# Performance work log

Hardware: AMD Instinct MI355X
Metric: run time of the kernel (lower is better)

Reference implementation:

```python
import jax, jax.numpy as jnp
import numpy as np

B, T, N, D, H, MH = 4, 16, 128, 16, 64, 128  # batch, timesteps, nodes, n_in_node, n_hid, msg_hid


def setup_inputs() -> dict:
    key = jax.random.key(0)
    ks = jax.random.split(key, 24)
    s = 0.1
    inp = {
        'A': jax.random.uniform(ks[0], (B, N, N), dtype=jnp.float32),
        'X': jax.random.normal(ks[1], (B, T, N, D), dtype=jnp.float32),
        'W_msg1': s * jax.random.normal(ks[2], (2 * H, MH), dtype=jnp.float32),
        'b_msg1': s * jax.random.normal(ks[3], (MH,), dtype=jnp.float32),
        'W_msg2': s * jax.random.normal(ks[4], (MH, H), dtype=jnp.float32),
        'b_msg2': s * jax.random.normal(ks[5], (H,), dtype=jnp.float32),
        'W_ir': s * jax.random.normal(ks[6], (D, H), dtype=jnp.float32),
        'b_ir': s * jax.random.normal(ks[7], (H,), dtype=jnp.float32),
        'W_ii': s * jax.random.normal(ks[8], (D, H), dtype=jnp.float32),
        'b_ii': s * jax.random.normal(ks[9], (H,), dtype=jnp.float32),
        'W_in': s * jax.random.normal(ks[10], (D, H), dtype=jnp.float32),
        'b_in': s * jax.random.normal(ks[11], (H,), dtype=jnp.float32),
        'W_hr': s * jax.random.normal(ks[12], (H, H), dtype=jnp.float32),
        'W_hi': s * jax.random.normal(ks[13], (H, H), dtype=jnp.float32),
        'W_hh': s * jax.random.normal(ks[14], (H, H), dtype=jnp.float32),
        'W_o1': s * jax.random.normal(ks[15], (H, H), dtype=jnp.float32),
        'b_o1': s * jax.random.normal(ks[16], (H,), dtype=jnp.float32),
        'W_o2': s * jax.random.normal(ks[17], (H, H), dtype=jnp.float32),
        'b_o2': s * jax.random.normal(ks[18], (H,), dtype=jnp.float32),
        'W_o3': s * jax.random.normal(ks[19], (H, D), dtype=jnp.float32),
        'b_o3': s * jax.random.normal(ks[20], (D,), dtype=jnp.float32),
        'log_sigma': jnp.log(jnp.float32(0.1)),
    }
    return inp


def reference(A, X, W_msg1, b_msg1, W_msg2, b_msg2, W_ir, b_ir, W_ii, b_ii,
              W_in, b_in, W_hr, W_hi, W_hh, W_o1, b_o1, W_o2, b_o2, W_o3,
              b_o3, log_sigma):
    Bv, Tv, Nv, Dv = X.shape
    Hv = W_hr.shape[0]
    # project_adjacency: symmetrize, zero diag, clamp to [0,1]
    A = (A + jnp.swapaxes(A, -1, -2)) * 0.5
    A = A * (1.0 - jnp.eye(Nv, dtype=A.dtype))
    A = jnp.clip(A, 0.0, 1.0)
    # split msg_fc1 into sender / receiver halves (cat([senders, receivers]) @ W)
    W1s, W1r = W_msg1[:Hv], W_msg1[Hv:]

    def step(carry, xs):
        hidden, total = carry
        x_t, x_next = xs  # [B,N,D]
        # message passing on hidden state: msg1[b,i,j] = tanh(h_i@W1s + h_j@W1r + b)
        hs = hidden @ W1s                      # [B,N,MH] sender part
        hr = hidden @ W1r + b_msg1             # [B,N,MH] receiver part
        m1 = jnp.tanh(hs[:, :, None, :] + hr[:, None, :, :])  # [B,N,N,MH]
        msg = jnp.tanh(m1 @ W_msg2 + b_msg2)   # [B,N,N,H]
        # weight by soft adjacency, sum over senders i -> agg at receiver j
        agg = jnp.einsum('bij,bijh->bjh', A, msg)  # [B,N,H]
        # GRU-style gating
        r = jax.nn.sigmoid(x_t @ W_ir + b_ir + agg @ W_hr)
        i = jax.nn.sigmoid(x_t @ W_ii + b_ii + agg @ W_hi)
        n = jnp.tanh(x_t @ W_in + b_in + r * (agg @ W_hh))
        hidden_new = (1.0 - i) * n + i * hidden
        # output MLP with residual
        p1 = jax.nn.relu(hidden_new @ W_o1 + b_o1)
        p2 = jax.nn.relu(p1 @ W_o2 + b_o2)
        pred = x_t + (p2 @ W_o3 + b_o3)
        # gaussian log-likelihood
        sigma = jnp.exp(log_sigma)
        mse = jnp.sum((x_next - pred) ** 2)
        const = Nv * Dv * Bv * jnp.log(sigma * jnp.sqrt(2.0 * jnp.pi))
        total = total - (mse / (2.0 * sigma ** 2) + const)
        return (hidden_new, total), pred

    hidden0 = jnp.zeros((Bv, Nv, Hv), dtype=X.dtype)
    xs = (jnp.swapaxes(X[:, :-1], 0, 1), jnp.swapaxes(X[:, 1:], 0, 1))  # time-major
    (_, loglik), preds = jax.lax.scan(step, (hidden0, jnp.float32(0.0)), xs)
    X_pred = jnp.swapaxes(preds, 0, 1)  # [B, T-1, N, D]
    return X_pred, loglik
```

## Files before the change

### kernel.cpp

```cpp
#include <hip/hip_runtime.h>

#define NBLK 512
#define CSCALE 2.8853900817779268f

#define OFF_HS   0
#define OFF_PART 65536
#define OFF_SYNC 66048
#define OFF_BF   66560

#define BW2F  0
#define BWIR  8192
#define BWII  9216
#define BWIN  10240
#define BWHR  11264
#define BWHI  15360
#define BWHH  19456
#define BWO1  23552
#define BWO2  27648
#define BWO3  31744
#define BW1S  32768
#define BW1RT 49152

#define INIT_TOTAL (32768 + 512 + 49152 + 8192)

typedef __attribute__((ext_vector_type(8))) __bf16 bf16x8;
typedef __attribute__((ext_vector_type(4))) float f32x4;
union frag_u { bf16x8 v; unsigned short s[8]; int4 q; };
union ldu { int4 q; unsigned short s[8]; unsigned u[4]; };

__device__ __forceinline__ unsigned short f2b(float x) {
  unsigned int u = __float_as_uint(x);
  u += 0x7fffu + ((u >> 16) & 1u);
  return (unsigned short)(u >> 16);
}
__device__ __forceinline__ float b2f(unsigned short u) {
  return __uint_as_float(((unsigned int)u) << 16);
}
__device__ __forceinline__ float fast_tanh(float x) {
  float e = __builtin_amdgcn_exp2f(x * CSCALE);
  return 1.0f - 2.0f * __builtin_amdgcn_rcpf(e + 1.0f);
}
__device__ __forceinline__ float tanh_pre(float x) {
  float e = __builtin_amdgcn_exp2f(x);
  return 1.0f - 2.0f * __builtin_amdgcn_rcpf(e + 1.0f);
}
__device__ __forceinline__ float fast_sigmoid(float x) {
  float e = __builtin_amdgcn_exp2f(x * -1.4426950408889634f);
  return __builtin_amdgcn_rcpf(1.0f + e);
}
__device__ __forceinline__ unsigned pack_bf2(float lo, float hi) {
  unsigned a = __float_as_uint(lo) + 0x8000u;
  unsigned b = __float_as_uint(hi) + 0x8000u;
  return __builtin_amdgcn_perm(b, a, 0x07060302u);
}
__device__ __forceinline__ void st_coh_u32(unsigned* p, unsigned v) {
  __hip_atomic_store(p, v, __ATOMIC_RELAXED, __HIP_MEMORY_SCOPE_AGENT);
}
__device__ __forceinline__ void st_coh_i32(int* p, int v) {
  __hip_atomic_store(p, v, __ATOMIC_RELAXED, __HIP_MEMORY_SCOPE_AGENT);
}

__global__ void init_kernel(const float* __restrict__ W_msg2,
                            const float* __restrict__ W_ir, const float* __restrict__ W_ii,
                            const float* __restrict__ W_in,
                            const float* __restrict__ W_hr, const float* __restrict__ W_hi,
                            const float* __restrict__ W_hh,
                            const float* __restrict__ W_o1, const float* __restrict__ W_o2,
                            const float* __restrict__ W_o3,
                            const float* __restrict__ W_msg1, float* __restrict__ ws) {
  int idx = blockIdx.x * 256 + threadIdx.x;
  unsigned short* bw = (unsigned short*)(ws + OFF_BF);
  if (idx < 32768) { ws[OFF_HS + idx] = 0.0f; return; }
  idx -= 32768;
  if (idx < 512) { ((int*)(ws + OFF_SYNC))[idx] = 0; return; }
  idx -= 512;
  if (idx < 8192) {
    int f = idx >> 9, l = (idx >> 3) & 63, jj = idx & 7;
    int kc = f >> 2, nt = f & 3;
    int k = kc * 32 + ((l >> 4) << 3) + jj;
    int n = (nt << 4) + (l & 15);
    bw[BW2F + idx] = f2b(W_msg2[k * 64 + n] * CSCALE);
    return;
  }
  idx -= 8192;
  if (idx < 1024) { bw[BWIR + idx] = f2b(W_ir[idx]); return; }
  idx -= 1024;
  if (idx < 1024) { bw[BWII + idx] = f2b(W_ii[idx]); return; }
  idx -= 1024;
  if (idx < 1024) { bw[BWIN + idx] = f2b(W_in[idx]); return; }
  idx -= 1024;
  if (idx < 4096) { bw[BWHR + idx] = f2b(W_hr[idx]); return; }
  idx -= 4096;
  if (idx < 4096) { bw[BWHI + idx] = f2b(W_hi[idx]); return; }
  idx -= 4096;
  if (idx < 4096) { bw[BWHH + idx] = f2b(W_hh[idx]); return; }
  idx -= 4096;
  if (idx < 4096) { bw[BWO1 + idx] = f2b(W_o1[idx]); return; }
  idx -= 4096;
  if (idx < 4096) { bw[BWO2 + idx] = f2b(W_o2[idx]); return; }
  idx -= 4096;
  if (idx < 1024) { bw[BWO3 + idx] = f2b(W_o3[idx]); return; }
  idx -= 1024;
  if (idx < 16384) { bw[BW1S + idx] = f2b(W_msg1[idx]); return; }
  idx -= 16384;
  if (idx < 8192) {
    int m = idx >> 6, h = idx & 63;
    bw[BW1RT + idx] = f2b(W_msg1[(64 + h) * 128 + m]);
    return;
  }
}

__launch_bounds__(256, 2)
__global__ void step_all_kernel(const float* __restrict__ A, const float* __restrict__ X,
                                const float* __restrict__ b_msg1, const float* __restrict__ b_msg2,
                                const float* __restrict__ b_ir, const float* __restrict__ b_ii,
                                const float* __restrict__ b_in,
                                const float* __restrict__ b_o1, const float* __restrict__ b_o2,
                                const float* __restrict__ b_o3,
                                float* __restrict__ ws, float* __restrict__ out) {
  const int tid = threadIdx.x;
  const int bj = blockIdx.x;
  const int b = bj >> 7, j = bj & 127;
  const int wave = tid >> 6, lane = tid & 63;
  const unsigned short* bw = (const unsigned short*)(ws + OFF_BF);
  unsigned short* hs16 = (unsigned short*)(ws + OFF_HS);
  int* flags = (int*)(ws + OFF_SYNC);

  __shared__ __align__(16) unsigned short lds_gate_t[3 * 64 * 68];
  __shared__ __align__(16) unsigned short lds_w1t[128 * 68];
  __shared__ __align__(16) unsigned short lds_outt[2 * 64 * 68 + 16 * 68];
  __shared__ __align__(16) float sh_hr[128];
  __shared__ __align__(16) float sh_Ar[128];
  __shared__ __align__(16) float sh_aggw[4][64];
  __shared__ __align__(16) float sh_agg[64];
  __shared__ __align__(16) float sh_xall[256];
  __shared__ __align__(16) float sh_hid[64];
  __shared__ __align__(16) float sh_pre[4][64];
  __shared__ int sh_w01;

  for (int i = tid; i < 12288; i += 256) {
    int g = i >> 12, r = i & 4095, k = r >> 6, h = r & 63;
    lds_gate_t[g * 4352 + h * 68 + k] = bw[BWHR + i];
  }
  for (int i = tid; i < 8192; i += 256) {
    int h = i >> 7, m = i & 127;
    lds_w1t[m * 68 + h] = bw[BW1S + i];
  }
  for (int i = tid; i < 8192; i += 256) {
    int o = i >> 12, r = i & 4095, k = r >> 6, h = r & 63;
    lds_outt[o * 4352 + h * 68 + k] = bw[BWO1 + i];
  }
  for (int i = tid; i < 1024; i += 256) {
    int k = i >> 4, d = i & 15;
    lds_outt[8704 + d * 68 + k] = bw[BWO3 + i];
  }
  {
    int t0 = tid >> 4, d = tid & 15;
    sh_xall[tid] = X[(((b << 4) + t0) << 11) + (j << 4) + d];
  }
  if (tid < 128) {
    float a1 = A[(b << 14) + (j << 7) + tid];
    float a2 = A[(b << 14) + (tid << 7) + j];
    float v = 0.5f * (a1 + a2);
    v = (tid == j) ? 0.0f : v;
    sh_Ar[tid] = fminf(fmaxf(v, 0.0f), 1.0f);
    sh_hr[tid] = b_msg1[tid] * CSCALE;
  } else if (tid < 192) {
    sh_hid[tid - 128] = 0.0f;
  }
  if (tid == 0) sh_w01 = 0;

  frag_u Bf[16];
  const int4* bw2 = (const int4*)bw;
#pragma unroll
  for (int f = 0; f < 16; ++f) Bf[f].q = bw2[f * 64 + lane];
  float b2v[4];
#pragma unroll
  for (int nt = 0; nt < 4; ++nt) b2v[nt] = b_msg2[nt * 16 + (lane & 15)] * CSCALE;
  float my_bias = 0.0f;
  float wx[16];
  if (wave != 2) {
    my_bias = (wave == 0) ? b_ir[lane] : (wave == 1) ? b_ii[lane] : b_in[lane];
    const int xo = (wave == 0) ? BWIR : (wave == 1) ? BWII : BWIN;
#pragma unroll
    for (int d = 0; d < 16; ++d) wx[d] = b2f(bw[xo + d * 64 + lane]);
  }
  const float bm1a = b_msg1[lane], bm1b = b_msg1[lane + 64];
  const float bo1 = b_o1[lane], bo2 = b_o2[lane];
  const float bo3 = (lane < 16) ? b_o3[lane] : 0.0f;
  float macc = 0.0f;

  const int lane15 = lane & 15;
  const int k0 = (lane >> 4) << 3;
  __syncthreads();

  for (int t = 0; t < 15; ++t) {
    const int par = t & 1;
    const unsigned short* hs_cur = hs16 + par * 65536;
    unsigned short* hs_nxt = hs16 + (par ^ 1) * 65536;

    ldu va[8];
    {
      const unsigned short* p0 = hs_cur + (((b << 7) + (wave << 5) + lane15) << 7) + k0;
      const unsigned short* p1 = p0 + 2048;
      asm volatile(
          "global_load_dwordx4 %0, %8, off sc0 sc1\n\t"
          "global_load_dwordx4 %1, %8, off offset:64 sc0 sc1\n\t"
          "global_load_dwordx4 %2, %8, off offset:128 sc0 sc1\n\t"
          "global_load_dwordx4 %3, %8, off offset:192 sc0 sc1\n\t"
          "global_load_dwordx4 %4, %9, off sc0 sc1\n\t"
          "global_load_dwordx4 %5, %9, off offset:64 sc0 sc1\n\t"
          "global_load_dwordx4 %6, %9, off offset:128 sc0 sc1\n\t"
          "global_load_dwordx4 %7, %9, off offset:192 sc0 sc1\n\t"
          "s_waitcnt vmcnt(0)"
          : "=&v"(va[0].q), "=&v"(va[1].q), "=&v"(va[2].q), "=&v"(va[3].q),
            "=&v"(va[4].q), "=&v"(va[5].q), "=&v"(va[6].q), "=&v"(va[7].q)
          : "v"(p0), "v"(p1)
          : "memory");
    }

    float part[4] = {0.f, 0.f, 0.f, 0.f};
#pragma unroll
    for (int c = 0; c < 2; ++c) {
      f32x4 acc[4];
#pragma unroll
      for (int nt = 0; nt < 4; ++nt) acc[nt] = (f32x4){0.f, 0.f, 0.f, 0.f};
#pragma unroll
      for (int kc = 0; kc < 4; ++kc) {
        const ldu& u = va[c * 4 + kc];
        const float* hp = sh_hr + kc * 32 + k0;
        frag_u Af;
        int* ap = (int*)&Af.q;
#pragma unroll
        for (int p = 0; p < 4; ++p) {
          unsigned w = u.u[p];
          float x0 = __uint_as_float(w << 16) + hp[2 * p];
          float x1 = __uint_as_float(w & 0xffff0000u) + hp[2 * p + 1];
          ap[p] = (int)pack_bf2(tanh_pre(x0), tanh_pre(x1));
        }
#pragma unroll
        for (int nt = 0; nt < 4; ++nt)
          acc[nt] = __builtin_amdgcn_mfma_f32_16x16x32_bf16(Af.v, Bf[kc * 4 + nt].v, acc[nt], 0, 0, 0);
      }
      const int ibase = ((wave << 1) + c) << 4;
      float4 aw = *(const float4*)(sh_Ar + ibase + ((lane >> 4) << 2));
#pragma unroll
      for (int r = 0; r < 4; ++r) {
        float wv = (r == 0) ? aw.x : (r == 1) ? aw.y : (r == 2) ? aw.z : aw.w;
#pragma unroll
        for (int nt = 0; nt < 4; ++nt)
          part[nt] += wv * tanh_pre(acc[nt][r] + b2v[nt]);
      }
    }
#pragma unroll
    for (int nt = 0; nt < 4; ++nt) {
      part[nt] += __shfl_xor(part[nt], 16);
      part[nt] += __shfl_xor(part[nt], 32);
    }
    if (lane < 16) {
#pragma unroll
      for (int nt = 0; nt < 4; ++nt) sh_aggw[wave][nt * 16 + lane] = part[nt];
    }
    __syncthreads();
    if (tid < 64)
      sh_agg[tid] = sh_aggw[0][tid] + sh_aggw[1][tid] + sh_aggw[2][tid] + sh_aggw[3][tid];
    __syncthreads();

    {
      float s = 0.0f;
      if (wave != 2) {
        s = my_bias;
        const float4* xr = (const float4*)(sh_xall + (t << 4));
#pragma unroll
        for (int c = 0; c < 4; ++c) {
          float4 xv = xr[c];
          s += xv.x * wx[4 * c] + xv.y * wx[4 * c + 1] + xv.z * wx[4 * c + 2] + xv.w * wx[4 * c + 3];
        }
      }
      if (wave != 3) {
        const ushort4* row = (const ushort4*)(lds_gate_t + wave * 4352 + lane * 68);
        const float4* ag = (const float4*)sh_agg;
        float a0 = s, a1 = 0.f, a2 = 0.f, a3 = 0.f;
#pragma unroll
        for (int c = 0; c < 16; ++c) {
          ushort4 wv = row[c];
          float4 av = ag[c];
          a0 += av.x * b2f(wv.x); a1 += av.y * b2f(wv.y);
          a2 += av.z * b2f(wv.z); a3 += av.w * b2f(wv.w);
        }
        s = (a0 + a1) + (a2 + a3);
      }
      sh_pre[wave][lane] = s;
    }
    __syncthreads();
    if (tid < 64) {
      float r  = fast_sigmoid(sh_pre[0][tid]);
      float ig = fast_sigmoid(sh_pre[1][tid]);
      float n  = fast_tanh(sh_pre[3][tid] + r * sh_pre[2][tid]);
      sh_hid[tid] = (1.0f - ig) * n + ig * sh_hid[tid];
    }
    __syncthreads();

    if (wave == 3) {
      const float4* h4 = (const float4*)sh_hid;
      {
        const ushort4* r1 = (const ushort4*)(lds_outt + lane * 68);
        float a0 = bo1, a1 = 0.f, a2 = 0.f, a3 = 0.f;
#pragma unroll
        for (int c = 0; c < 16; ++c) {
          ushort4 wv = r1[c]; float4 hv = h4[c];
          a0 += hv.x * b2f(wv.x); a1 += hv.y * b2f(wv.y);
          a2 += hv.z * b2f(wv.z); a3 += hv.w * b2f(wv.w);
        }
        sh_pre[0][lane] = fmaxf((a0 + a1) + (a2 + a3), 0.0f);
      }
      {
        const ushort4* r2 = (const ushort4*)(lds_outt + 4352 + lane * 68);
        const float4* p4 = (const float4*)sh_pre[0];
        float a0 = bo2, a1 = 0.f, a2 = 0.f, a3 = 0.f;
#pragma unroll
        for (int c = 0; c < 16; ++c) {
          ushort4 wv = r2[c]; float4 pv = p4[c];
          a0 += pv.x * b2f(wv.x); a1 += pv.y * b2f(wv.y);
          a2 += pv.z * b2f(wv.z); a3 += pv.w * b2f(wv.w);
        }
        sh_pre[1][lane] = fmaxf((a0 + a1) + (a2 + a3), 0.0f);
      }
      if (lane < 16) {
        const ushort4* r3 = (const ushort4*)(lds_outt + 8704 + lane * 68);
        const float4* q4 = (const float4*)sh_pre[1];
        float a0 = bo3, a1 = 0.f, a2 = 0.f, a3 = 0.f;
#pragma unroll
        for (int c = 0; c < 16; ++c) {
          ushort4 wv = r3[c]; float4 qv = q4[c];
          a0 += qv.x * b2f(wv.x); a1 += qv.y * b2f(wv.y);
          a2 += qv.z * b2f(wv.z); a3 += qv.w * b2f(wv.w);
        }
        float pred = sh_xall[(t << 4) + lane] + (a0 + a1) + (a2 + a3);
        out[((b * 15 + t) * 128 + j) * 16 + lane] = pred;
        float d = sh_xall[((t + 1) << 4) + lane] - pred;
        macc += d * d;
      }
    } else if (t < 14) {
      if (wave <= 1) {
        const int m = tid;
        const ushort4* row = (const ushort4*)(lds_w1t + m * 68);
        const float4* h4 = (const float4*)sh_hid;
        float a0 = 0.f, a1 = 0.f, a2 = 0.f, a3 = 0.f;
#pragma unroll
        for (int c = 0; c < 16; ++c) {
          ushort4 wv = row[c]; float4 hv = h4[c];
          a0 += hv.x * b2f(wv.x); a1 += hv.y * b2f(wv.y);
          a2 += hv.z * b2f(wv.z); a3 += hv.w * b2f(wv.w);
        }
        float s = ((a0 + a1) + (a2 + a3)) * CSCALE;
        float hi = __shfl_down(s, 1);
        if (!(lane & 1))
          st_coh_u32((unsigned*)hs_nxt + (bj << 6) + (m >> 1), pack_bf2(s, hi));
        asm volatile("s_waitcnt vmcnt(0)" ::: "memory");
        if (lane == 0) atomicAdd(&sh_w01, 1);
        if (wave == 0) {
          const int tgt = t + 1;
          if (lane == 0) {
            while (__hip_atomic_load(&sh_w01, __ATOMIC_RELAXED, __HIP_MEMORY_SCOPE_WORKGROUP) < 2 * tgt) {}
            st_coh_i32(flags + (b << 7) + j, tgt);
          }
          const int* fp = flags + (b << 7) + (lane << 1);
          int2 fv;
          do {
            asm volatile("global_load_dwordx2 %0, %1, off sc0 sc1\n\ts_waitcnt vmcnt(0)"
                         : "=v"(fv) : "v"(fp) : "memory");
          } while (__any(fv.x < tgt || fv.y < tgt));
        }
      } else {
        const int4* wp1 = (const int4*)(bw + BW1RT + (lane << 6));
        const int4* wp2 = (const int4*)(bw + BW1RT + ((lane + 64) << 6));
        const float4* h4 = (const float4*)sh_hid;
        float s1a = bm1a, s1b = 0.f, s2a = bm1b, s2b = 0.f;
#pragma unroll
        for (int c = 0; c < 8; ++c) {
          ldu u1, u2; u1.q = wp1[c]; u2.q = wp2[c];
          float4 h0 = h4[2 * c], h1 = h4[2 * c + 1];
          s1a += h0.x * b2f(u1.s[0]); s1b += h0.y * b2f(u1.s[1]);
          s1a += h0.z * b2f(u1.s[2]); s1b += h0.w * b2f(u1.s[3]);
          s1a += h1.x * b2f(u1.s[4]); s1b += h1.y * b2f(u1.s[5]);
          s1a += h1.z * b2f(u1.s[6]); s1b += h1.w * b2f(u1.s[7]);
          s2a += h0.x * b2f(u2.s[0]); s2b += h0.y * b2f(u2.s[1]);
          s2a += h0.z * b2f(u2.s[2]); s2b += h0.w * b2f(u2.s[3]);
          s2a += h1.x * b2f(u2.s[4]); s2b += h1.y * b2f(u2.s[5]);
          s2a += h1.z * b2f(u2.s[6]); s2b += h1.w * b2f(u2.s[7]);
        }
        sh_hr[lane] = (s1a + s1b) * CSCALE;
        sh_hr[lane + 64] = (s2a + s2b) * CSCALE;
      }
    }
    __syncthreads();
  }

  if (wave == 3) {
    macc += __shfl_xor(macc, 1);
    macc += __shfl_xor(macc, 2);
    macc += __shfl_xor(macc, 4);
    macc += __shfl_xor(macc, 8);
    if (lane == 0) ws[OFF_PART + bj] = macc;
  }
}

__global__ void final_kernel(const float* __restrict__ log_sigma, const float* __restrict__ ws,
                             float* __restrict__ out) {
  __shared__ float red[256];
  const int tid = threadIdx.x;
  red[tid] = ws[OFF_PART + tid] + ws[OFF_PART + 256 + tid];
  __syncthreads();
  if (tid == 0) {
    float mse = 0.0f;
    for (int i = 0; i < 256; ++i) mse += red[i];
    float sigma = expf(log_sigma[0]);
    float cst = 8192.0f * logf(sigma * sqrtf(6.2831853071795864f));
    out[122880] = -(mse / (2.0f * sigma * sigma) + 15.0f * cst);
  }
}

extern "C" void kernel_launch(void* const* d_in, const int* in_sizes, int n_in,
                              void* d_out, int out_size, void* d_ws, size_t ws_size,
                              hipStream_t stream) {
  (void)in_sizes; (void)n_in; (void)out_size; (void)ws_size;
  const float* A      = (const float*)d_in[0];
  const float* X      = (const float*)d_in[1];
  const float* W_msg1 = (const float*)d_in[2];
  const float* b_msg1 = (const float*)d_in[3];
  const float* W_msg2 = (const float*)d_in[4];
  const float* b_msg2 = (const float*)d_in[5];
  const float* W_ir   = (const float*)d_in[6];
  const float* b_ir   = (const float*)d_in[7];
  const float* W_ii   = (const float*)d_in[8];
  const float* b_ii   = (const float*)d_in[9];
  const float* W_in   = (const float*)d_in[10];
  const float* b_in   = (const float*)d_in[11];
  const float* W_hr   = (const float*)d_in[12];
  const float* W_hi   = (const float*)d_in[13];
  const float* W_hh   = (const float*)d_in[14];
  const float* W_o1   = (const float*)d_in[15];
  const float* b_o1   = (const float*)d_in[16];
  const float* W_o2   = (const float*)d_in[17];
  const float* b_o2   = (const float*)d_in[18];
  const float* W_o3   = (const float*)d_in[19];
  const float* b_o3   = (const float*)d_in[20];
  const float* log_sigma = (const float*)d_in[21];
  float* ws  = (float*)d_ws;
  float* out = (float*)d_out;

  init_kernel<<<(INIT_TOTAL + 255) / 256, 256, 0, stream>>>(
      W_msg2, W_ir, W_ii, W_in, W_hr, W_hi, W_hh, W_o1, W_o2, W_o3, W_msg1, ws);
  step_all_kernel<<<NBLK, 256, 0, stream>>>(A, X, b_msg1, b_msg2, b_ir, b_ii, b_in,
                                            b_o1, b_o2, b_o3, ws, out);
  final_kernel<<<1, 256, 0, stream>>>(log_sigma, ws, out);
}
```

Before: 262.9 us.

## Defer output MLP to after recurrence and move flag polling to idle wave

The output MLP, which does not feed the recurrence, is moved out of the per-timestep loop. Hidden states are saved in a shared history buffer and all four waves compute the output MLP for the 15 timesteps after the loop. Cross-block flag polling moves from wave 0 to wave 3, which is now idle during the step. Weight LDS layouts change from padded row-major to an interleaved chunk layout so that lanes read consecutive ushort4 values. The critical path of each step gets shorter, at the cost of 3.8KB more LDS and an extra block reduction at the end.

```diff
diff --git a/kernel.cpp b/kernel.cpp
--- a/kernel.cpp
+++ b/kernel.cpp
@@ -126,33 +126,34 @@
   unsigned short* hs16 = (unsigned short*)(ws + OFF_HS);
   int* flags = (int*)(ws + OFF_SYNC);
 
-  __shared__ __align__(16) unsigned short lds_gate_t[3 * 64 * 68];
-  __shared__ __align__(16) unsigned short lds_w1t[128 * 68];
-  __shared__ __align__(16) unsigned short lds_outt[2 * 64 * 68 + 16 * 68];
+  __shared__ __align__(16) unsigned short lds_gate_t[12288];
+  __shared__ __align__(16) unsigned short lds_w1t[8192];
+  __shared__ __align__(16) unsigned short lds_outt[9216];
   __shared__ __align__(16) float sh_hr[128];
   __shared__ __align__(16) float sh_Ar[128];
   __shared__ __align__(16) float sh_aggw[4][64];
   __shared__ __align__(16) float sh_agg[64];
   __shared__ __align__(16) float sh_xall[256];
   __shared__ __align__(16) float sh_hid[64];
+  __shared__ __align__(16) float sh_hist[960];
   __shared__ __align__(16) float sh_pre[4][64];
   __shared__ int sh_w01;
 
   for (int i = tid; i < 12288; i += 256) {
-    int g = i >> 12, r = i & 4095, k = r >> 6, h = r & 63;
-    lds_gate_t[g * 4352 + h * 68 + k] = bw[BWHR + i];
+    int g = i >> 12, r = i & 4095, c = r >> 8, rem = r & 255, h = rem >> 2, s = rem & 3;
+    lds_gate_t[i] = bw[BWHR + (g << 12) + (((c << 2) + s) << 6) + h];
   }
   for (int i = tid; i < 8192; i += 256) {
-    int h = i >> 7, m = i & 127;
-    lds_w1t[m * 68 + h] = bw[BW1S + i];
+    int c = i >> 9, rem = i & 511, m = rem >> 2, s = rem & 3;
+    lds_w1t[i] = bw[BW1S + (((c << 2) + s) << 7) + m];
   }
   for (int i = tid; i < 8192; i += 256) {
-    int o = i >> 12, r = i & 4095, k = r >> 6, h = r & 63;
-    lds_outt[o * 4352 + h * 68 + k] = bw[BWO1 + i];
+    int o = i >> 12, r = i & 4095, c = r >> 8, rem = r & 255, h = rem >> 2, s = rem & 3;
+    lds_outt[i] = bw[BWO1 + (o << 12) + (((c << 2) + s) << 6) + h];
   }
   for (int i = tid; i < 1024; i += 256) {
-    int k = i >> 4, d = i & 15;
-    lds_outt[8704 + d * 68 + k] = bw[BWO3 + i];
+    int c = i >> 6, rem = i & 63, d = rem >> 2, s = rem & 3;
+    lds_outt[8192 + i] = bw[BWO3 + (((c << 2) + s) << 4) + d];
   }
   {
     int t0 = tid >> 4, d = tid & 15;
@@ -278,12 +279,12 @@
         }
       }
       if (wave != 3) {
-        const ushort4* row = (const ushort4*)(lds_gate_t + wave * 4352 + lane * 68);
+        const ushort4* gp = ((const ushort4*)lds_gate_t) + (wave << 10) + lane;
         const float4* ag = (const float4*)sh_agg;
         float a0 = s, a1 = 0.f, a2 = 0.f, a3 = 0.f;
 #pragma unroll
         for (int c = 0; c < 16; ++c) {
-          ushort4 wv = row[c];
+          ushort4 wv = gp[c << 6];
           float4 av = ag[c];
           a0 += av.x * b2f(wv.x); a1 += av.y * b2f(wv.y);
           a2 += av.z * b2f(wv.z); a3 += av.w * b2f(wv.w);
@@ -297,59 +298,22 @@
       float r  = fast_sigmoid(sh_pre[0][tid]);
       float ig = fast_sigmoid(sh_pre[1][tid]);
       float n  = fast_tanh(sh_pre[3][tid] + r * sh_pre[2][tid]);
-      sh_hid[tid] = (1.0f - ig) * n + ig * sh_hid[tid];
+      float hnew = (1.0f - ig) * n + ig * sh_hid[tid];
+      sh_hid[tid] = hnew;
+      sh_hist[t * 64 + tid] = hnew;
     }
     __syncthreads();
 
-    if (wave == 3) {
-      const float4* h4 = (const float4*)sh_hid;
-      {
-        const ushort4* r1 = (const ushort4*)(lds_outt + lane * 68);
-        float a0 = bo1, a1 = 0.f, a2 = 0.f, a3 = 0.f;
-#pragma unroll
-        for (int c = 0; c < 16; ++c) {
-          ushort4 wv = r1[c]; float4 hv = h4[c];
-          a0 += hv.x * b2f(wv.x); a1 += hv.y * b2f(wv.y);
-          a2 += hv.z * b2f(wv.z); a3 += hv.w * b2f(wv.w);
-        }
-        sh_pre[0][lane] = fmaxf((a0 + a1) + (a2 + a3), 0.0f);
-      }
-      {
-        const ushort4* r2 = (const ushort4*)(lds_outt + 4352 + lane * 68);
-        const float4* p4 = (const float4*)sh_pre[0];
-        float a0 = bo2, a1 = 0.f, a2 = 0.f, a3 = 0.f;
-#pragma unroll
-        for (int c = 0; c < 16; ++c) {
-          ushort4 wv = r2[c]; float4 pv = p4[c];
-          a0 += pv.x * b2f(wv.x); a1 += pv.y * b2f(wv.y);
-          a2 += pv.z * b2f(wv.z); a3 += pv.w * b2f(wv.w);
-        }
-        sh_pre[1][lane] = fmaxf((a0 + a1) + (a2 + a3), 0.0f);
-      }
-      if (lane < 16) {
-        const ushort4* r3 = (const ushort4*)(lds_outt + 8704 + lane * 68);
-        const float4* q4 = (const float4*)sh_pre[1];
-        float a0 = bo3, a1 = 0.f, a2 = 0.f, a3 = 0.f;
-#pragma unroll
-        for (int c = 0; c < 16; ++c) {
-          ushort4 wv = r3[c]; float4 qv = q4[c];
-          a0 += qv.x * b2f(wv.x); a1 += qv.y * b2f(wv.y);
-          a2 += qv.z * b2f(wv.z); a3 += qv.w * b2f(wv.w);
-        }
-        float pred = sh_xall[(t << 4) + lane] + (a0 + a1) + (a2 + a3);
-        out[((b * 15 + t) * 128 + j) * 16 + lane] = pred;
-        float d = sh_xall[((t + 1) << 4) + lane] - pred;
-        macc += d * d;
-      }
-    } else if (t < 14) {
+    if (t < 14) {
       if (wave <= 1) {
         const int m = tid;
-        const ushort4* row = (const ushort4*)(lds_w1t + m * 68);
+        const ushort4* wp = ((const ushort4*)lds_w1t) + m;
         const float4* h4 = (const float4*)sh_hid;
         float a0 = 0.f, a1 = 0.f, a2 = 0.f, a3 = 0.f;
 #pragma unroll
         for (int c = 0; c < 16; ++c) {
-          ushort4 wv = row[c]; float4 hv = h4[c];
+          ushort4 wv = wp[c << 7];
+          float4 hv = h4[c];
           a0 += hv.x * b2f(wv.x); a1 += hv.y * b2f(wv.y);
           a2 += hv.z * b2f(wv.z); a3 += hv.w * b2f(wv.w);
         }
@@ -359,20 +323,12 @@
           st_coh_u32((unsigned*)hs_nxt + (bj << 6) + (m >> 1), pack_bf2(s, hi));
         asm volatile("s_waitcnt vmcnt(0)" ::: "memory");
         if (lane == 0) atomicAdd(&sh_w01, 1);
-        if (wave == 0) {
-          const int tgt = t + 1;
-          if (lane == 0) {
-            while (__hip_atomic_load(&sh_w01, __ATOMIC_RELAXED, __HIP_MEMORY_SCOPE_WORKGROUP) < 2 * tgt) {}
-            st_coh_i32(flags + (b << 7) + j, tgt);
-          }
-          const int* fp = flags + (b << 7) + (lane << 1);
-          int2 fv;
-          do {
-            asm volatile("global_load_dwordx2 %0, %1, off sc0 sc1\n\ts_waitcnt vmcnt(0)"
-                         : "=v"(fv) : "v"(fp) : "memory");
-          } while (__any(fv.x < tgt || fv.y < tgt));
-        }
-      } else {
+        if (wave == 0 && lane == 0) {
+          const int tgt2 = 2 * (t + 1);
+          while (__hip_atomic_load(&sh_w01, __ATOMIC_RELAXED, __HIP_MEMORY_SCOPE_WORKGROUP) < tgt2) {}
+          st_coh_i32(flags + (b << 7) + j, t + 1);
+        }
+      } else if (wave == 2) {
         const int4* wp1 = (const int4*)(bw + BW1RT + (lane << 6));
         const int4* wp2 = (const int4*)(bw + BW1RT + ((lane + 64) << 6));
         const float4* h4 = (const float4*)sh_hid;
@@ -392,18 +348,71 @@
         }
         sh_hr[lane] = (s1a + s1b) * CSCALE;
         sh_hr[lane + 64] = (s2a + s2b) * CSCALE;
+      } else {
+        const int tgt = t + 1;
+        const int* fp = flags + (b << 7) + (lane << 1);
+        int2 fv;
+        do {
+          asm volatile("global_load_dwordx2 %0, %1, off sc0 sc1\n\ts_waitcnt vmcnt(0)"
+                       : "=v"(fv) : "v"(fp) : "memory");
+        } while (__any(fv.x < tgt || fv.y < tgt));
       }
     }
     __syncthreads();
   }
 
-  if (wave == 3) {
-    macc += __shfl_xor(macc, 1);
-    macc += __shfl_xor(macc, 2);
-    macc += __shfl_xor(macc, 4);
-    macc += __shfl_xor(macc, 8);
-    if (lane == 0) ws[OFF_PART + bj] = macc;
-  }
+#pragma unroll
+  for (int it = 0; it < 4; ++it) {
+    const int tt = wave + it * 4;
+    if (tt >= 15) continue;
+    const float4* h4 = (const float4*)(sh_hist + tt * 64);
+    {
+      const ushort4* r1 = ((const ushort4*)lds_outt) + lane;
+      float a0 = bo1, a1 = 0.f, a2 = 0.f, a3 = 0.f;
+#pragma unroll
+      for (int c = 0; c < 16; ++c) {
+        ushort4 wv = r1[c << 6]; float4 hv = h4[c];
+        a0 += hv.x * b2f(wv.x); a1 += hv.y * b2f(wv.y);
+        a2 += hv.z * b2f(wv.z); a3 += hv.w * b2f(wv.w);
+      }
+      sh_pre[wave][lane] = fmaxf((a0 + a1) + (a2 + a3), 0.0f);
+    }
+    {
+      const ushort4* r2 = ((const ushort4*)lds_outt) + 1024 + lane;
+      const float4* p4 = (const float4*)sh_pre[wave];
+      float a0 = bo2, a1 = 0.f, a2 = 0.f, a3 = 0.f;
+#pragma unroll
+      for (int c = 0; c < 16; ++c) {
+        ushort4 wv = r2[c << 6]; float4 pv = p4[c];
+        a0 += pv.x * b2f(wv.x); a1 += pv.y * b2f(wv.y);
+        a2 += pv.z * b2f(wv.z); a3 += pv.w * b2f(wv.w);
+      }
+      sh_aggw[wave][lane] = fmaxf((a0 + a1) + (a2 + a3), 0.0f);
+    }
+    if (lane < 16) {
+      const ushort4* r3 = ((const ushort4*)lds_outt) + 2048 + lane;
+      const float4* q4 = (const float4*)sh_aggw[wave];
+      float a0 = bo3, a1 = 0.f, a2 = 0.f, a3 = 0.f;
+#pragma unroll
+      for (int c = 0; c < 16; ++c) {
+        ushort4 wv = r3[c << 4]; float4 qv = q4[c];
+        a0 += qv.x * b2f(wv.x); a1 += qv.y * b2f(wv.y);
+        a2 += qv.z * b2f(wv.z); a3 += qv.w * b2f(wv.w);
+      }
+      float pred = sh_xall[(tt << 4) + lane] + (a0 + a1) + (a2 + a3);
+      out[((b * 15 + tt) * 128 + j) * 16 + lane] = pred;
+      float d = sh_xall[((tt + 1) << 4) + lane] - pred;
+      macc += d * d;
+    }
+  }
+  macc += __shfl_xor(macc, 1);
+  macc += __shfl_xor(macc, 2);
+  macc += __shfl_xor(macc, 4);
+  macc += __shfl_xor(macc, 8);
+  __syncthreads();
+  if (lane == 0) sh_agg[wave] = macc;
+  __syncthreads();
+  if (tid == 0) ws[OFF_PART + bj] = sh_agg[0] + sh_agg[1] + sh_agg[2] + sh_agg[3];
 }
 
 __global__ void final_kernel(const float* __restrict__ log_sigma, const float* __restrict__ ws,
```

New measurement: 282.1 us. +7.3%, slower.
